# Optimization experiments

Hardware: AMD Instinct MI355X
Metric: run time of the kernel (lower is better)

Reference implementation:

```python
import jax, jax.numpy as jnp
import numpy as np

N_NODES = 50000
N_EDGES = 600000
F_IN = 128
HID = 128
N_CLASSES = 10


def _gcn_graph(edge_index, n_nodes):
    # PyG GCNConv: add self-loops, deg computed on target (col) with weight 1,
    # norm_e = deg^-1/2[src] * deg^-1/2[dst]
    src = jnp.concatenate([edge_index[0], jnp.arange(n_nodes, dtype=edge_index.dtype)])
    dst = jnp.concatenate([edge_index[1], jnp.arange(n_nodes, dtype=edge_index.dtype)])
    deg = jax.ops.segment_sum(jnp.ones_like(dst, dtype=jnp.float32), dst, num_segments=n_nodes)
    dinv = jnp.where(deg > 0, jax.lax.rsqrt(deg), 0.0)
    norm = dinv[src] * dinv[dst]  # [E+N]
    return src, dst, norm


def _gcn_layer(x, W, b, src, dst, norm, n_nodes):
    h = x @ W                      # [N, out] linear first (bias applied post-agg)
    m = h[src] * norm[:, None]     # gather + scale, [E+N, out]
    out = jax.ops.segment_sum(m, dst, num_segments=n_nodes)  # scatter-add
    return out + b


def setup_inputs() -> dict:
    key = jax.random.key(0)
    ks = jax.random.split(key, 4)
    x = jax.random.normal(ks[0], (N_NODES, F_IN), dtype=jnp.float32)
    edge_index = jax.random.randint(ks[1], (2, N_EDGES), 0, N_NODES, dtype=jnp.int64)
    # Glorot-ish init scale for weights
    W_stack = jax.random.normal(ks[2], (8, HID, HID), dtype=jnp.float32) * (1.0 / np.sqrt(HID))
    b_stack = jnp.zeros((8, HID), dtype=jnp.float32)
    W_out = jax.random.normal(ks[3], (HID, N_CLASSES), dtype=jnp.float32) * (1.0 / np.sqrt(HID))
    b_out = jnp.zeros((N_CLASSES,), dtype=jnp.float32)
    return {"x": x, "edge_index": edge_index, "W_stack": W_stack, "b_stack": b_stack,
            "W_out": W_out, "b_out": b_out}


def reference(x, edge_index, W_stack, b_stack, W_out, b_out):
    n_nodes = x.shape[0]
    src, dst, norm = _gcn_graph(edge_index, n_nodes)
    h = x
    for i in range(8):  # conv1..conv8 with ELU
        h = jax.nn.elu(_gcn_layer(h, W_stack[i], b_stack[i], src, dst, norm, n_nodes))
    # conv9: no activation
    return _gcn_layer(h, W_out, b_out, src, dst, norm, n_nodes)
```

## Files before the change

### kernel.cpp

```cpp
#include <hip/hip_runtime.h>
#include <math.h>

#define NN 50000
#define NE 600000
#define HID 128
#define NCLS 10
#define T2S 16

typedef __bf16 bf16x8 __attribute__((ext_vector_type(8)));
typedef float f32x16 __attribute__((ext_vector_type(16)));

__device__ __forceinline__ void split3(float f, ushort& h, ushort& m, ushort& l) {
    unsigned uh = __float_as_uint(f) & 0xffff0000u;
    float fm = f - __uint_as_float(uh);
    unsigned um = __float_as_uint(fm) & 0xffff0000u;
    float fl = fm - __uint_as_float(um);
    h = (ushort)(uh >> 16);
    m = (ushort)(um >> 16);
    l = (ushort)(__float_as_uint(fl) >> 16);
}


__global__ __launch_bounds__(256) void k_count(const int* __restrict__ edge,
                                               int* __restrict__ counts) {
    int e = blockIdx.x * 256 + threadIdx.x;
    if (e < NE) atomicAdd(&counts[edge[NE + e]], 1);
}

__device__ __forceinline__ int wave_incl_scan(int x, int lane) {
#pragma unroll
    for (int off = 1; off < 64; off <<= 1) {
        int y = __shfl_up(x, off, 64);
        if (lane >= off) x += y;
    }
    return x;
}

__global__ __launch_bounds__(256) void k_scan1(const int* __restrict__ counts,
                                               int* __restrict__ rowptr,
                                               int* __restrict__ bsum,
                                               float* __restrict__ dinv) {
    __shared__ int ws[4];
    int tid = threadIdx.x;
    int i = blockIdx.x * 256 + tid;
    int lane = tid & 63, wv = tid >> 6;
    int v = (i < NN) ? counts[i] : 0;
    if (i < NN) dinv[i] = rsqrtf((float)(v + 1));
    int x = wave_incl_scan(v, lane);
    if (lane == 63) ws[wv] = x;
    __syncthreads();
    int off = 0;
    for (int j = 0; j < wv; ++j) off += ws[j];
    if (i < NN) rowptr[i] = off + x - v;
    if (tid == 255) bsum[blockIdx.x] = off + x;
}

__global__ __launch_bounds__(256) void k_scan2(int* __restrict__ bsum, int n) {
    __shared__ int ws[4];
    int tid = threadIdx.x;
    int lane = tid & 63, wv = tid >> 6;
    int v = (tid < n) ? bsum[tid] : 0;
    int x = wave_incl_scan(v, lane);
    if (lane == 63) ws[wv] = x;
    __syncthreads();
    int off = 0;
    for (int j = 0; j < wv; ++j) off += ws[j];
    __syncthreads();
    if (tid < n) bsum[tid] = off + x - v;
}

__global__ __launch_bounds__(256) void k_scan3(int* __restrict__ rowptr,
                                               const int* __restrict__ bsum) {
    int i = blockIdx.x * 256 + threadIdx.x;
    if (i < NN) rowptr[i] += bsum[blockIdx.x];
    if (i == 0) rowptr[NN] = NE;
}

__global__ __launch_bounds__(256) void k_fill(const int* __restrict__ edge,
                                              const int* __restrict__ rowptr,
                                              int* __restrict__ cursor,
                                              const float* __restrict__ dinv,
                                              int2* __restrict__ csr) {
    int e = blockIdx.x * 256 + threadIdx.x;
    if (e >= NE) return;
    int s = edge[e], d = edge[NE + e];
    int slot = atomicSub(&cursor[d], 1) - 1;
    csr[rowptr[d] + slot] = make_int2(s, __float_as_int(dinv[s] * dinv[d]));
}


__global__ __launch_bounds__(256) void k_split_w(const float* __restrict__ Wst,
                                                 ushort* __restrict__ Wt4) {
    int i = blockIdx.x * 256 + threadIdx.x;
    if (i >= 8 * HID * HID) return;
    int l = i >> 14;
    int k = (i >> 7) & 127;
    int n = i & 127;
    ushort h, m, lo;
    split3(Wst[i], h, m, lo);
    int ks = k >> 4, r = k & 15;
    size_t base = ((((size_t)l * 3) * 8 + ks) * 128 + n) * 16 + r;
    const size_t pstride = (size_t)8 * 128 * 16;
    Wt4[base] = h;
    Wt4[base + pstride] = m;
    Wt4[base + 2 * pstride] = lo;
}


__global__ __launch_bounds__(256) void k_mfma_gemm(const float* __restrict__ H,
                                                   const ushort* __restrict__ Wt,
                                                   float* __restrict__ T) {
    int tid = threadIdx.x;
    int lane = tid & 63, w = tid >> 6;
    int l31 = lane & 31, lh = lane >> 5;
    int rowbase = blockIdx.x * 128;

    int grow = rowbase + w * 32 + l31;
    if (grow >= NN) grow = NN - 1;
    const float* arow = H + (size_t)grow * HID + lh * 8;
    const ushort* wbase = Wt + (size_t)l31 * 16 + lh * 8;

    f32x16 acc[4] = {};

#pragma unroll 2
    for (int s = 0; s < 8; ++s) {
        const float4* ap = (const float4*)(arow + s * 16);
        float4 f0 = ap[0], f1 = ap[1];
        float av[8] = {f0.x, f0.y, f0.z, f0.w, f1.x, f1.y, f1.z, f1.w};
        union { ushort u[8]; bf16x8 v; } ah, am, al;
#pragma unroll
        for (int q = 0; q < 8; ++q) split3(av[q], ah.u[q], am.u[q], al.u[q]);

        uint4 bf[3][4];
#pragma unroll
        for (int p = 0; p < 3; ++p)
#pragma unroll
            for (int c = 0; c < 4; ++c)
                bf[p][c] = *(const uint4*)(wbase + (((size_t)p * 8 + s) * 128 + c * 32) * 16);

#pragma unroll
        for (int c = 0; c < 4; ++c)
            acc[c] = __builtin_amdgcn_mfma_f32_32x32x16_bf16(ah.v, *(const bf16x8*)&bf[0][c], acc[c], 0, 0, 0);
#pragma unroll
        for (int c = 0; c < 4; ++c)
            acc[c] = __builtin_amdgcn_mfma_f32_32x32x16_bf16(ah.v, *(const bf16x8*)&bf[1][c], acc[c], 0, 0, 0);
#pragma unroll
        for (int c = 0; c < 4; ++c)
            acc[c] = __builtin_amdgcn_mfma_f32_32x32x16_bf16(am.v, *(const bf16x8*)&bf[0][c], acc[c], 0, 0, 0);
#pragma unroll
        for (int c = 0; c < 4; ++c)
            acc[c] = __builtin_amdgcn_mfma_f32_32x32x16_bf16(ah.v, *(const bf16x8*)&bf[2][c], acc[c], 0, 0, 0);
#pragma unroll
        for (int c = 0; c < 4; ++c)
            acc[c] = __builtin_amdgcn_mfma_f32_32x32x16_bf16(am.v, *(const bf16x8*)&bf[1][c], acc[c], 0, 0, 0);
#pragma unroll
        for (int c = 0; c < 4; ++c)
            acc[c] = __builtin_amdgcn_mfma_f32_32x32x16_bf16(al.v, *(const bf16x8*)&bf[0][c], acc[c], 0, 0, 0);
    }

#pragma unroll
    for (int c = 0; c < 4; ++c)
#pragma unroll
        for (int reg = 0; reg < 16; ++reg) {
            int r = (reg & 3) + 8 * (reg >> 2) + 4 * lh;
            int gr = rowbase + w * 32 + r;
            if (gr < NN)
                T[(size_t)gr * HID + c * 32 + l31] = acc[c][reg];
        }
}

__device__ __forceinline__ void gather2_to_lds(const float* __restrict__ Tin,
                                               const int* __restrict__ rowptr,
                                               const int2* __restrict__ csr,
                                               const float* __restrict__ dinv,
                                               float4 bv, float* Hs,
                                               int rowbase, int w, int h, int l31) {
    int lrow = w * 16 + h;
    int node = rowbase + lrow;
    if (node >= NN) node = NN - 1;
    int beg = rowptr[node], end = rowptr[node + 1];
    float sn = dinv[node];
    float4 tv = ((const float4*)(Tin + (size_t)node * HID))[l31];

    for (int i = 0; i < 8; ++i) {
        int nlrow = lrow + 2;
        int nbeg = 0, nend = 0;
        float nsn = 0.f;
        float4 ntv = {0.f, 0.f, 0.f, 0.f};
        if (i < 7) {
            int nnode = rowbase + nlrow;
            if (nnode >= NN) nnode = NN - 1;
            nbeg = rowptr[nnode];
            nend = rowptr[nnode + 1];
            nsn = dinv[nnode];
            ntv = ((const float4*)(Tin + (size_t)nnode * HID))[l31];
        }

        float s2 = sn * sn;
        float4 acc;
        acc.x = s2 * tv.x + bv.x;
        acc.y = s2 * tv.y + bv.y;
        acc.z = s2 * tv.z + bv.z;
        acc.w = s2 * tv.w + bv.w;

        const int2 zed = make_int2(0, 0);
        int p = beg;
        int2 e0 = (p < end) ? csr[p] : zed;
        int2 e1 = (p + 1 < end) ? csr[p + 1] : zed;
        int2 e2 = (p + 2 < end) ? csr[p + 2] : zed;
        int2 e3 = (p + 3 < end) ? csr[p + 3] : zed;
        for (; p < end; p += 4) {
            float4 u0 = ((const float4*)(Tin + (size_t)e0.x * HID))[l31];
            float4 u1 = ((const float4*)(Tin + (size_t)e1.x * HID))[l31];
            float4 u2 = ((const float4*)(Tin + (size_t)e2.x * HID))[l31];
            float4 u3 = ((const float4*)(Tin + (size_t)e3.x * HID))[l31];
            float w0 = __int_as_float(e0.y), w1 = __int_as_float(e1.y);
            float w2 = __int_as_float(e2.y), w3 = __int_as_float(e3.y);
            e0 = (p + 4 < end) ? csr[p + 4] : zed;
            e1 = (p + 5 < end) ? csr[p + 5] : zed;
            e2 = (p + 6 < end) ? csr[p + 6] : zed;
            e3 = (p + 7 < end) ? csr[p + 7] : zed;
            acc.x += w0 * u0.x; acc.y += w0 * u0.y; acc.z += w0 * u0.z; acc.w += w0 * u0.w;
            acc.x += w1 * u1.x; acc.y += w1 * u1.y; acc.z += w1 * u1.z; acc.w += w1 * u1.w;
            acc.x += w2 * u2.x; acc.y += w2 * u2.y; acc.z += w2 * u2.z; acc.w += w2 * u2.w;
            acc.x += w3 * u3.x; acc.y += w3 * u3.y; acc.z += w3 * u3.z; acc.w += w3 * u3.w;
        }

        acc.x = acc.x > 0.f ? acc.x : expm1f(acc.x);
        acc.y = acc.y > 0.f ? acc.y : expm1f(acc.y);
        acc.z = acc.z > 0.f ? acc.z : expm1f(acc.z);
        acc.w = acc.w > 0.f ? acc.w : expm1f(acc.w);
        int byte = lrow * 512 + l31 * 16;
        byte ^= (lrow & 7) << 4;
        *(float4*)((char*)Hs + byte) = acc;

        lrow = nlrow; beg = nbeg; end = nend; sn = nsn; tv = ntv;
    }
}


__global__ __launch_bounds__(256, 4) void k_fused(const float* __restrict__ Tin,
                                                  const ushort* __restrict__ Wt,
                                                  const int* __restrict__ rowptr,
                                                  const int2* __restrict__ csr,
                                                  const float* __restrict__ dinv,
                                                  const float* __restrict__ bias,
                                                  float* __restrict__ Tout) {
    __shared__ float Hs[64 * 128];
    int tid = threadIdx.x;
    int lane = tid & 63, w = tid >> 6;
    int hh = lane >> 5, l31 = lane & 31;
    int rowbase = blockIdx.x * 64;

    float4 bv = ((const float4*)bias)[l31];

    gather2_to_lds(Tin, rowptr, csr, dinv, bv, Hs, rowbase, w, hh, l31);
    __syncthreads();

    int lh = hh;
    int rloc = (w >> 1) * 32 + l31;
    int colh = w & 1;
    const ushort* wbase = Wt + ((size_t)(colh * 64) + l31) * 16 + lh * 8;

    f32x16 acc2[2] = {};

#pragma unroll 2
    for (int s = 0; s < 8; ++s) {
        int byte = rloc * 512 + s * 64 + lh * 32;
        int sw = (rloc & 7) << 4;
        float4 f0 = *(const float4*)((const char*)Hs + (byte ^ sw));
        float4 f1 = *(const float4*)((const char*)Hs + ((byte + 16) ^ sw));
        float av[8] = {f0.x, f0.y, f0.z, f0.w, f1.x, f1.y, f1.z, f1.w};
        union { ushort u[8]; bf16x8 v; } ah, am, al;
#pragma unroll
        for (int q = 0; q < 8; ++q) split3(av[q], ah.u[q], am.u[q], al.u[q]);

        uint4 bf[3][2];
#pragma unroll
        for (int p = 0; p < 3; ++p)
#pragma unroll
            for (int c = 0; c < 2; ++c)
                bf[p][c] = *(const uint4*)(wbase + (((size_t)p * 8 + s) * 128 + c * 32) * 16);

#pragma unroll
        for (int c = 0; c < 2; ++c)
            acc2[c] = __builtin_amdgcn_mfma_f32_32x32x16_bf16(ah.v, *(const bf16x8*)&bf[0][c], acc2[c], 0, 0, 0);
#pragma unroll
        for (int c = 0; c < 2; ++c)
            acc2[c] = __builtin_amdgcn_mfma_f32_32x32x16_bf16(ah.v, *(const bf16x8*)&bf[1][c], acc2[c], 0, 0, 0);
#pragma unroll
        for (int c = 0; c < 2; ++c)
            acc2[c] = __builtin_amdgcn_mfma_f32_32x32x16_bf16(am.v, *(const bf16x8*)&bf[0][c], acc2[c], 0, 0, 0);
#pragma unroll
        for (int c = 0; c < 2; ++c)
            acc2[c] = __builtin_amdgcn_mfma_f32_32x32x16_bf16(ah.v, *(const bf16x8*)&bf[2][c], acc2[c], 0, 0, 0);
#pragma unroll
        for (int c = 0; c < 2; ++c)
            acc2[c] = __builtin_amdgcn_mfma_f32_32x32x16_bf16(am.v, *(const bf16x8*)&bf[1][c], acc2[c], 0, 0, 0);
#pragma unroll
        for (int c = 0; c < 2; ++c)
            acc2[c] = __builtin_amdgcn_mfma_f32_32x32x16_bf16(al.v, *(const bf16x8*)&bf[0][c], acc2[c], 0, 0, 0);
    }

#pragma unroll
    for (int c = 0; c < 2; ++c)
#pragma unroll
        for (int reg = 0; reg < 16; ++reg) {
            int r = (reg & 3) + 8 * (reg >> 2) + 4 * lh;
            int gr = rowbase + (w >> 1) * 32 + r;
            if (gr < NN)
                Tout[(size_t)gr * HID + colh * 64 + c * 32 + l31] = acc2[c][reg];
        }
}


__global__ __launch_bounds__(256, 4) void k_fused_out(const float* __restrict__ Tin,
                                                      const float* __restrict__ W,
                                                      const int* __restrict__ rowptr,
                                                      const int2* __restrict__ csr,
                                                      const float* __restrict__ dinv,
                                                      const float* __restrict__ bias,
                                                      float* __restrict__ T2) {
    __shared__ float Hs[64 * 128];
    __shared__ float Ws[128 * 11];
    int tid = threadIdx.x;
    int lane = tid & 63, w = tid >> 6;
    int hh = lane >> 5, l31 = lane & 31;
    int rowbase = blockIdx.x * 64;

    for (int m = tid; m < HID * NCLS; m += 256) {
        int k = m / NCLS, c = m - k * NCLS;
        Ws[k * 11 + c] = W[m];
    }

    float4 bv = ((const float4*)bias)[l31];
    gather2_to_lds(Tin, rowptr, csr, dinv, bv, Hs, rowbase, w, hh, l31);
    __syncthreads();

    int row = tid >> 2;
    int t4 = tid & 3;
    float acc[NCLS];
#pragma unroll
    for (int c = 0; c < NCLS; ++c) acc[c] = 0.f;
    int sw = (row & 7) << 4;
#pragma unroll
    for (int q = 0; q < 8; ++q) {
        int c16 = q * 4 + t4;
        float4 f = *(const float4*)((const char*)Hs + ((row * 512 + c16 * 16) ^ sw));
        float hv[4] = {f.x, f.y, f.z, f.w};
#pragma unroll
        for (int j = 0; j < 4; ++j) {
            const float* wr = &Ws[(c16 * 4 + j) * 11];
#pragma unroll
            for (int c = 0; c < NCLS; ++c) acc[c] += hv[j] * wr[c];
        }
    }
#pragma unroll
    for (int off = 2; off >= 1; off >>= 1) {
#pragma unroll
        for (int c = 0; c < NCLS; ++c) acc[c] += __shfl_xor(acc[c], off, 4);
    }
    int gr = rowbase + row;
    if (t4 == 0 && gr < NN) {
#pragma unroll
        for (int c = 0; c < NCLS; ++c) T2[(size_t)gr * T2S + c] = acc[c];
    }
}

__global__ __launch_bounds__(256) void k_gather_out(const float* __restrict__ T2,
                                                    float* __restrict__ out,
                                                    const int* __restrict__ rowptr,
                                                    const int2* __restrict__ csr,
                                                    const float* __restrict__ dinv,
                                                    const float* __restrict__ bias) {
    int lane = threadIdx.x & 63;
    int node = (blockIdx.x * 256 + threadIdx.x) >> 6;
    if (node >= NN) return;
    int slot = lane >> 4, c = lane & 15;
    int beg = rowptr[node], end = rowptr[node + 1];
    float acc = 0.f;
    if (c < NCLS) {
        for (int i = beg + slot; i < end; i += 4) {
            int2 e = csr[i];
            acc += __int_as_float(e.y) * T2[(size_t)e.x * T2S + c];
        }
    }
    acc += __shfl_xor(acc, 16, 64);
    acc += __shfl_xor(acc, 32, 64);
    if (slot == 0 && c < NCLS) {
        float sn = dinv[node];
        sn *= sn;
        out[node * NCLS + c] = acc + sn * T2[(size_t)node * T2S + c] + bias[c];
    }
}


extern "C" void kernel_launch(void* const* d_in, const int* in_sizes, int n_in,
                              void* d_out, int out_size, void* d_ws, size_t ws_size,
                              hipStream_t stream) {
    (void)in_sizes; (void)n_in; (void)out_size; (void)ws_size;
    const float* x       = (const float*)d_in[0];
    const int*   edge    = (const int*)d_in[1];
    const float* W_stack = (const float*)d_in[2];
    const float* b_stack = (const float*)d_in[3];
    const float* W_out   = (const float*)d_in[4];
    const float* b_out   = (const float*)d_in[5];
    float* out = (float*)d_out;

    char* ws = (char*)d_ws;
    const size_t bigbuf = (size_t)NN * HID * sizeof(float);
    float* X      = (float*)ws;
    float* Y      = (float*)(ws + bigbuf);
    char*  p      = ws + 2 * bigbuf;
    int2*  csr    = (int2*)p;              p += sizeof(int2) * NE;
    float* dinv   = (float*)p;             p += sizeof(float) * NN;
    int*   rowptr = (int*)p;               p += sizeof(int) * (NN + 1);
    int*   counts = (int*)p;               p += sizeof(int) * NN;
    int*   bsum   = (int*)p;               p += sizeof(int) * 256;
    p = (char*)(((size_t)p + 15) & ~(size_t)15);
    ushort* Wt4 = (ushort*)p;  p += sizeof(ushort) * 8 * 3 * HID * HID;
    float* T2b  = (float*)p;   p += sizeof(float) * NN * T2S;

    const int NB_N  = (NN + 255) / 256;
    const int NB_E  = (NE + 255) / 256;
    const int NB_G  = (NN + 127) / 128;
    const int NB_F  = (NN + 63) / 64;
    const int NB_A  = (NN * 64 + 255) / 256;
    const int NB_SW = (8 * HID * HID + 255) / 256;

    hipMemsetAsync(counts, 0, sizeof(int) * NN, stream);
    k_count<<<NB_E, 256, 0, stream>>>(edge, counts);
    k_scan1<<<NB_N, 256, 0, stream>>>(counts, rowptr, bsum, dinv);
    k_scan2<<<1, 256, 0, stream>>>(bsum, NB_N);
    k_scan3<<<NB_N, 256, 0, stream>>>(rowptr, bsum);
    k_fill<<<NB_E, 256, 0, stream>>>(edge, rowptr, counts, dinv, csr);

    k_split_w<<<NB_SW, 256, 0, stream>>>(W_stack, Wt4);

    k_mfma_gemm<<<NB_G, 256, 0, stream>>>(x, Wt4, Y);

    float* cur = Y;
    float* nxt = X;
    for (int l = 0; l < 7; ++l) {
        k_fused<<<NB_F, 256, 0, stream>>>(cur, Wt4 + (size_t)(l + 1) * 3 * HID * HID,
                                          rowptr, csr, dinv,
                                          b_stack + (size_t)l * HID, nxt);
        float* t = cur; cur = nxt; nxt = t;
    }

    k_fused_out<<<NB_F, 256, 0, stream>>>(cur, W_out, rowptr, csr, dinv,
                                          b_stack + (size_t)7 * HID, T2b);

    k_gather_out<<<NB_A, 256, 0, stream>>>(T2b, out, rowptr, csr, dinv, b_out);
}
```

Before: 649.6 us.

## Fuse all GCN layers into one cooperative persistent kernel with grid syncs

Replaces the chain of per-layer launches (first GEMM, seven fused gather+GEMM layers, output layer, final gather) with a single cooperative kernel of 782 blocks that uses grid.sync between layers. The first GEMM is re-tiled to 64-row tiles to match the fused layout. The goal is to remove kernel launch gaps and tail effects between the roughly ten dependent kernels. The cost is that cooperative launch needs all 782 blocks co-resident, which at 4 blocks per CU relies on register and LDS limits. If the launch fails, it falls back to the multi-kernel path.

New measurement: 1.617 ms. +148.9%, slower.

```diff
diff --git a/kernel.cpp b/kernel.cpp
--- a/kernel.cpp
+++ b/kernel.cpp
@@ -1,11 +1,15 @@
 #include <hip/hip_runtime.h>
+#include <hip/hip_cooperative_groups.h>
 #include <math.h>
+
+namespace cg = cooperative_groups;
 
 #define NN 50000
 #define NE 600000
 #define HID 128
 #define NCLS 10
 #define T2S 16
+#define NBF 782
 
 typedef __bf16 bf16x8 __attribute__((ext_vector_type(8)));
 typedef float f32x16 __attribute__((ext_vector_type(16)));
@@ -106,68 +110,6 @@
     Wt4[base + 2 * pstride] = lo;
 }
 
-
-__global__ __launch_bounds__(256) void k_mfma_gemm(const float* __restrict__ H,
-                                                   const ushort* __restrict__ Wt,
-                                                   float* __restrict__ T) {
-    int tid = threadIdx.x;
-    int lane = tid & 63, w = tid >> 6;
-    int l31 = lane & 31, lh = lane >> 5;
-    int rowbase = blockIdx.x * 128;
-
-    int grow = rowbase + w * 32 + l31;
-    if (grow >= NN) grow = NN - 1;
-    const float* arow = H + (size_t)grow * HID + lh * 8;
-    const ushort* wbase = Wt + (size_t)l31 * 16 + lh * 8;
-
-    f32x16 acc[4] = {};
-
-#pragma unroll 2
-    for (int s = 0; s < 8; ++s) {
-        const float4* ap = (const float4*)(arow + s * 16);
-        float4 f0 = ap[0], f1 = ap[1];
-        float av[8] = {f0.x, f0.y, f0.z, f0.w, f1.x, f1.y, f1.z, f1.w};
-        union { ushort u[8]; bf16x8 v; } ah, am, al;
-#pragma unroll
-        for (int q = 0; q < 8; ++q) split3(av[q], ah.u[q], am.u[q], al.u[q]);
-
-        uint4 bf[3][4];
-#pragma unroll
-        for (int p = 0; p < 3; ++p)
-#pragma unroll
-            for (int c = 0; c < 4; ++c)
-                bf[p][c] = *(const uint4*)(wbase + (((size_t)p * 8 + s) * 128 + c * 32) * 16);
-
-#pragma unroll
-        for (int c = 0; c < 4; ++c)
-            acc[c] = __builtin_amdgcn_mfma_f32_32x32x16_bf16(ah.v, *(const bf16x8*)&bf[0][c], acc[c], 0, 0, 0);
-#pragma unroll
-        for (int c = 0; c < 4; ++c)
-            acc[c] = __builtin_amdgcn_mfma_f32_32x32x16_bf16(ah.v, *(const bf16x8*)&bf[1][c], acc[c], 0, 0, 0);
-#pragma unroll
-        for (int c = 0; c < 4; ++c)
-            acc[c] = __builtin_amdgcn_mfma_f32_32x32x16_bf16(am.v, *(const bf16x8*)&bf[0][c], acc[c], 0, 0, 0);
-#pragma unroll
-        for (int c = 0; c < 4; ++c)
-            acc[c] = __builtin_amdgcn_mfma_f32_32x32x16_bf16(ah.v, *(const bf16x8*)&bf[2][c], acc[c], 0, 0, 0);
-#pragma unroll
-        for (int c = 0; c < 4; ++c)
-            acc[c] = __builtin_amdgcn_mfma_f32_32x32x16_bf16(am.v, *(const bf16x8*)&bf[1][c], acc[c], 0, 0, 0);
-#pragma unroll
-        for (int c = 0; c < 4; ++c)
-            acc[c] = __builtin_amdgcn_mfma_f32_32x32x16_bf16(al.v, *(const bf16x8*)&bf[0][c], acc[c], 0, 0, 0);
-    }
-
-#pragma unroll
-    for (int c = 0; c < 4; ++c)
-#pragma unroll
-        for (int reg = 0; reg < 16; ++reg) {
-            int r = (reg & 3) + 8 * (reg >> 2) + 4 * lh;
-            int gr = rowbase + w * 32 + r;
-            if (gr < NN)
-                T[(size_t)gr * HID + c * 32 + l31] = acc[c][reg];
-        }
-}
 
 __device__ __forceinline__ void gather2_to_lds(const float* __restrict__ Tin,
                                                const int* __restrict__ rowptr,
@@ -238,6 +180,217 @@
     }
 }
 
+__device__ __forceinline__ void mfma_step(const float av[8],
+                                          const ushort* __restrict__ wbase,
+                                          int s, f32x16 acc2[2]) {
+    union { ushort u[8]; bf16x8 v; } ah, am, al;
+#pragma unroll
+    for (int q = 0; q < 8; ++q) split3(av[q], ah.u[q], am.u[q], al.u[q]);
+
+    uint4 bf[3][2];
+#pragma unroll
+    for (int p = 0; p < 3; ++p)
+#pragma unroll
+        for (int c = 0; c < 2; ++c)
+            bf[p][c] = *(const uint4*)(wbase + (((size_t)p * 8 + s) * 128 + c * 32) * 16);
+
+#pragma unroll
+    for (int c = 0; c < 2; ++c)
+        acc2[c] = __builtin_amdgcn_mfma_f32_32x32x16_bf16(ah.v, *(const bf16x8*)&bf[0][c], acc2[c], 0, 0, 0);
+#pragma unroll
+    for (int c = 0; c < 2; ++c)
+        acc2[c] = __builtin_amdgcn_mfma_f32_32x32x16_bf16(ah.v, *(const bf16x8*)&bf[1][c], acc2[c], 0, 0, 0);
+#pragma unroll
+    for (int c = 0; c < 2; ++c)
+        acc2[c] = __builtin_amdgcn_mfma_f32_32x32x16_bf16(am.v, *(const bf16x8*)&bf[0][c], acc2[c], 0, 0, 0);
+#pragma unroll
+    for (int c = 0; c < 2; ++c)
+        acc2[c] = __builtin_amdgcn_mfma_f32_32x32x16_bf16(ah.v, *(const bf16x8*)&bf[2][c], acc2[c], 0, 0, 0);
+#pragma unroll
+    for (int c = 0; c < 2; ++c)
+        acc2[c] = __builtin_amdgcn_mfma_f32_32x32x16_bf16(am.v, *(const bf16x8*)&bf[1][c], acc2[c], 0, 0, 0);
+#pragma unroll
+    for (int c = 0; c < 2; ++c)
+        acc2[c] = __builtin_amdgcn_mfma_f32_32x32x16_bf16(al.v, *(const bf16x8*)&bf[0][c], acc2[c], 0, 0, 0);
+}
+
+__device__ __forceinline__ void cstore(f32x16 acc2[2], float* __restrict__ Tout,
+                                       int rowbase, int w, int lh, int l31, int colh) {
+#pragma unroll
+    for (int c = 0; c < 2; ++c)
+#pragma unroll
+        for (int reg = 0; reg < 16; ++reg) {
+            int r = (reg & 3) + 8 * (reg >> 2) + 4 * lh;
+            int gr = rowbase + (w >> 1) * 32 + r;
+            if (gr < NN)
+                Tout[(size_t)gr * HID + colh * 64 + c * 32 + l31] = acc2[c][reg];
+        }
+}
+
+__device__ __forceinline__ void phase2_gemm(const float* Hs,
+                                            const ushort* __restrict__ Wt,
+                                            float* __restrict__ Tout,
+                                            int rowbase, int tid) {
+    int lane = tid & 63, w = tid >> 6;
+    int l31 = lane & 31, lh = lane >> 5;
+    int rloc = (w >> 1) * 32 + l31;
+    int colh = w & 1;
+    const ushort* wbase = Wt + ((size_t)(colh * 64) + l31) * 16 + lh * 8;
+
+    f32x16 acc2[2] = {};
+#pragma unroll 2
+    for (int s = 0; s < 8; ++s) {
+        int byte = rloc * 512 + s * 64 + lh * 32;
+        int sw = (rloc & 7) << 4;
+        float4 f0 = *(const float4*)((const char*)Hs + (byte ^ sw));
+        float4 f1 = *(const float4*)((const char*)Hs + ((byte + 16) ^ sw));
+        float av[8] = {f0.x, f0.y, f0.z, f0.w, f1.x, f1.y, f1.z, f1.w};
+        mfma_step(av, wbase, s, acc2);
+    }
+    cstore(acc2, Tout, rowbase, w, lh, l31, colh);
+}
+
+__device__ __forceinline__ void gemm0_tile(const float* __restrict__ x,
+                                           const ushort* __restrict__ Wt,
+                                           float* __restrict__ Tout,
+                                           int rowbase, int tid) {
+    int lane = tid & 63, w = tid >> 6;
+    int l31 = lane & 31, lh = lane >> 5;
+    int rloc = (w >> 1) * 32 + l31;
+    int colh = w & 1;
+    int grow = rowbase + rloc;
+    if (grow >= NN) grow = NN - 1;
+    const float* arow = x + (size_t)grow * HID + lh * 8;
+    const ushort* wbase = Wt + ((size_t)(colh * 64) + l31) * 16 + lh * 8;
+
+    f32x16 acc2[2] = {};
+#pragma unroll 2
+    for (int s = 0; s < 8; ++s) {
+        const float4* ap = (const float4*)(arow + s * 16);
+        float4 f0 = ap[0], f1 = ap[1];
+        float av[8] = {f0.x, f0.y, f0.z, f0.w, f1.x, f1.y, f1.z, f1.w};
+        mfma_step(av, wbase, s, acc2);
+    }
+    cstore(acc2, Tout, rowbase, w, lh, l31, colh);
+}
+
+__device__ __forceinline__ void fusedout_phase2(const float* Hs, const float* Ws,
+                                                float* __restrict__ T2,
+                                                int rowbase, int tid) {
+    int row = tid >> 2;
+    int t4 = tid & 3;
+    float acc[NCLS];
+#pragma unroll
+    for (int c = 0; c < NCLS; ++c) acc[c] = 0.f;
+    int sw = (row & 7) << 4;
+#pragma unroll
+    for (int q = 0; q < 8; ++q) {
+        int c16 = q * 4 + t4;
+        float4 f = *(const float4*)((const char*)Hs + ((row * 512 + c16 * 16) ^ sw));
+        float hv[4] = {f.x, f.y, f.z, f.w};
+#pragma unroll
+        for (int j = 0; j < 4; ++j) {
+            const float* wr = &Ws[(c16 * 4 + j) * 11];
+#pragma unroll
+            for (int c = 0; c < NCLS; ++c) acc[c] += hv[j] * wr[c];
+        }
+    }
+#pragma unroll
+    for (int off = 2; off >= 1; off >>= 1) {
+#pragma unroll
+        for (int c = 0; c < NCLS; ++c) acc[c] += __shfl_xor(acc[c], off, 4);
+    }
+    int gr = rowbase + row;
+    if (t4 == 0 && gr < NN) {
+#pragma unroll
+        for (int c = 0; c < NCLS; ++c) T2[(size_t)gr * T2S + c] = acc[c];
+    }
+}
+
+__device__ __forceinline__ void gatherout_body(const float* __restrict__ T2,
+                                               float* __restrict__ out,
+                                               const int* __restrict__ rowptr,
+                                               const int2* __restrict__ csr,
+                                               const float* __restrict__ dinv,
+                                               const float* __restrict__ bias,
+                                               int node, int lane) {
+    if (node >= NN) return;
+    int slot = lane >> 4, c = lane & 15;
+    int beg = rowptr[node], end = rowptr[node + 1];
+    float acc = 0.f;
+    if (c < NCLS) {
+        for (int i = beg + slot; i < end; i += 4) {
+            int2 e = csr[i];
+            acc += __int_as_float(e.y) * T2[(size_t)e.x * T2S + c];
+        }
+    }
+    acc += __shfl_xor(acc, 16, 64);
+    acc += __shfl_xor(acc, 32, 64);
+    if (slot == 0 && c < NCLS) {
+        float sn = dinv[node];
+        sn *= sn;
+        out[node * NCLS + c] = acc + sn * T2[(size_t)node * T2S + c] + bias[c];
+    }
+}
+
+
+__global__ __launch_bounds__(256, 4) void k_mega(const float* __restrict__ x,
+                                                 const ushort* __restrict__ Wt4,
+                                                 const float* __restrict__ W_out,
+                                                 const int* __restrict__ rowptr,
+                                                 const int2* __restrict__ csr,
+                                                 const float* __restrict__ dinv,
+                                                 const float* __restrict__ b_stack,
+                                                 const float* __restrict__ b_out,
+                                                 float* __restrict__ Y,
+                                                 float* __restrict__ X,
+                                                 float* __restrict__ T2b,
+                                                 float* __restrict__ out) {
+    __shared__ float Hs[64 * 128];
+    __shared__ float Ws[128 * 11];
+    cg::grid_group grid = cg::this_grid();
+    int tid = threadIdx.x;
+    int rowbase = blockIdx.x * 64;
+    int lane = tid & 63, w = tid >> 6;
+    int hh = lane >> 5, l31 = lane & 31;
+
+    gemm0_tile(x, Wt4, Y, rowbase, tid);
+    grid.sync();
+
+    float* cur = Y;
+    float* nxt = X;
+    for (int l = 0; l < 7; ++l) {
+        float4 bv = ((const float4*)(b_stack + (size_t)l * HID))[l31];
+        gather2_to_lds(cur, rowptr, csr, dinv, bv, Hs, rowbase, w, hh, l31);
+        __syncthreads();
+        phase2_gemm(Hs, Wt4 + (size_t)(l + 1) * 3 * HID * HID, nxt, rowbase, tid);
+        grid.sync();
+        float* t = cur; cur = nxt; nxt = t;
+    }
+
+    for (int m = tid; m < HID * NCLS; m += 256) {
+        int k = m / NCLS, c = m - k * NCLS;
+        Ws[k * 11 + c] = W_out[m];
+    }
+    {
+        float4 bv = ((const float4*)(b_stack + (size_t)7 * HID))[l31];
+        gather2_to_lds(cur, rowptr, csr, dinv, bv, Hs, rowbase, w, hh, l31);
+    }
+    __syncthreads();
+    fusedout_phase2(Hs, Ws, T2b, rowbase, tid);
+    grid.sync();
+
+    for (int base = blockIdx.x * 4; base < NN; base += NBF * 4) {
+        gatherout_body(T2b, out, rowptr, csr, dinv, b_out, base + (tid >> 6), lane);
+    }
+}
+
+
+__global__ __launch_bounds__(256) void k_gemm0(const float* __restrict__ x,
+                                               const ushort* __restrict__ Wt,
+                                               float* __restrict__ T) {
+    gemm0_tile(x, Wt, T, blockIdx.x * 64, threadIdx.x);
+}
 
 __global__ __launch_bounds__(256, 4) void k_fused(const float* __restrict__ Tin,
                                                   const ushort* __restrict__ Wt,
@@ -251,68 +404,11 @@
     int lane = tid & 63, w = tid >> 6;
     int hh = lane >> 5, l31 = lane & 31;
     int rowbase = blockIdx.x * 64;
-
     float4 bv = ((const float4*)bias)[l31];
-
     gather2_to_lds(Tin, rowptr, csr, dinv, bv, Hs, rowbase, w, hh, l31);
     __syncthreads();
-
-    int lh = hh;
-    int rloc = (w >> 1) * 32 + l31;
-    int colh = w & 1;
-    const ushort* wbase = Wt + ((size_t)(colh * 64) + l31) * 16 + lh * 8;
-
-    f32x16 acc2[2] = {};
-
-#pragma unroll 2
-    for (int s = 0; s < 8; ++s) {
-        int byte = rloc * 512 + s * 64 + lh * 32;
-        int sw = (rloc & 7) << 4;
-        float4 f0 = *(const float4*)((const char*)Hs + (byte ^ sw));
-        float4 f1 = *(const float4*)((const char*)Hs + ((byte + 16) ^ sw));
-        float av[8] = {f0.x, f0.y, f0.z, f0.w, f1.x, f1.y, f1.z, f1.w};
-        union { ushort u[8]; bf16x8 v; } ah, am, al;
-#pragma unroll
-        for (int q = 0; q < 8; ++q) split3(av[q], ah.u[q], am.u[q], al.u[q]);
-
-        uint4 bf[3][2];
-#pragma unroll
-        for (int p = 0; p < 3; ++p)
-#pragma unroll
-            for (int c = 0; c < 2; ++c)
-                bf[p][c] = *(const uint4*)(wbase + (((size_t)p * 8 + s) * 128 + c * 32) * 16);
-
-#pragma unroll
-        for (int c = 0; c < 2; ++c)
-            acc2[c] = __builtin_amdgcn_mfma_f32_32x32x16_bf16(ah.v, *(const bf16x8*)&bf[0][c], acc2[c], 0, 0, 0);
-#pragma unroll
-        for (int c = 0; c < 2; ++c)
-            acc2[c] = __builtin_amdgcn_mfma_f32_32x32x16_bf16(ah.v, *(const bf16x8*)&bf[1][c], acc2[c], 0, 0, 0);
-#pragma unroll
-        for (int c = 0; c < 2; ++c)
-            acc2[c] = __builtin_amdgcn_mfma_f32_32x32x16_bf16(am.v, *(const bf16x8*)&bf[0][c], acc2[c], 0, 0, 0);
-#pragma unroll
-        for (int c = 0; c < 2; ++c)
-            acc2[c] = __builtin_amdgcn_mfma_f32_32x32x16_bf16(ah.v, *(const bf16x8*)&bf[2][c], acc2[c], 0, 0, 0);
-#pragma unroll
-        for (int c = 0; c < 2; ++c)
-            acc2[c] = __builtin_amdgcn_mfma_f32_32x32x16_bf16(am.v, *(const bf16x8*)&bf[1][c], acc2[c], 0, 0, 0);
-#pragma unroll
-        for (int c = 0; c < 2; ++c)
-            acc2[c] = __builtin_amdgcn_mfma_f32_32x32x16_bf16(al.v, *(const bf16x8*)&bf[0][c], acc2[c], 0, 0, 0);
-    }
-
-#pragma unroll
-    for (int c = 0; c < 2; ++c)
-#pragma unroll
-        for (int reg = 0; reg < 16; ++reg) {
-            int r = (reg & 3) + 8 * (reg >> 2) + 4 * lh;
-            int gr = rowbase + (w >> 1) * 32 + r;
-            if (gr < NN)
-                Tout[(size_t)gr * HID + colh * 64 + c * 32 + l31] = acc2[c][reg];
-        }
-}
-
+    phase2_gemm(Hs, Wt, Tout, rowbase, tid);
+}
 
 __global__ __launch_bounds__(256, 4) void k_fused_out(const float* __restrict__ Tin,
                                                       const float* __restrict__ W,
@@ -327,44 +423,14 @@
     int lane = tid & 63, w = tid >> 6;
     int hh = lane >> 5, l31 = lane & 31;
     int rowbase = blockIdx.x * 64;
-
     for (int m = tid; m < HID * NCLS; m += 256) {
         int k = m / NCLS, c = m - k * NCLS;
         Ws[k * 11 + c] = W[m];
     }
-
     float4 bv = ((const float4*)bias)[l31];
     gather2_to_lds(Tin, rowptr, csr, dinv, bv, Hs, rowbase, w, hh, l31);
     __syncthreads();
-
-    int row = tid >> 2;
-    int t4 = tid & 3;
-    float acc[NCLS];
-#pragma unroll
-    for (int c = 0; c < NCLS; ++c) acc[c] = 0.f;
-    int sw = (row & 7) << 4;
-#pragma unroll
-    for (int q = 0; q < 8; ++q) {
-        int c16 = q * 4 + t4;
-        float4 f = *(const float4*)((const char*)Hs + ((row * 512 + c16 * 16) ^ sw));
-        float hv[4] = {f.x, f.y, f.z, f.w};
-#pragma unroll
-        for (int j = 0; j < 4; ++j) {
-            const float* wr = &Ws[(c16 * 4 + j) * 11];
-#pragma unroll
-            for (int c = 0; c < NCLS; ++c) acc[c] += hv[j] * wr[c];
-        }
-    }
-#pragma unroll
-    for (int off = 2; off >= 1; off >>= 1) {
-#pragma unroll
-        for (int c = 0; c < NCLS; ++c) acc[c] += __shfl_xor(acc[c], off, 4);
-    }
-    int gr = rowbase + row;
-    if (t4 == 0 && gr < NN) {
-#pragma unroll
-        for (int c = 0; c < NCLS; ++c) T2[(size_t)gr * T2S + c] = acc[c];
-    }
+    fusedout_phase2(Hs, Ws, T2, rowbase, tid);
 }
 
 __global__ __launch_bounds__(256) void k_gather_out(const float* __restrict__ T2,
@@ -375,23 +441,7 @@
                                                     const float* __restrict__ bias) {
     int lane = threadIdx.x & 63;
     int node = (blockIdx.x * 256 + threadIdx.x) >> 6;
-    if (node >= NN) return;
-    int slot = lane >> 4, c = lane & 15;
-    int beg = rowptr[node], end = rowptr[node + 1];
-    float acc = 0.f;
-    if (c < NCLS) {
-        for (int i = beg + slot; i < end; i += 4) {
-            int2 e = csr[i];
-            acc += __int_as_float(e.y) * T2[(size_t)e.x * T2S + c];
-        }
-    }
-    acc += __shfl_xor(acc, 16, 64);
-    acc += __shfl_xor(acc, 32, 64);
-    if (slot == 0 && c < NCLS) {
-        float sn = dinv[node];
-        sn *= sn;
-        out[node * NCLS + c] = acc + sn * T2[(size_t)node * T2S + c] + bias[c];
-    }
+    gatherout_body(T2, out, rowptr, csr, dinv, bias, node, lane);
 }
 
 
@@ -423,8 +473,6 @@
 
     const int NB_N  = (NN + 255) / 256;
     const int NB_E  = (NE + 255) / 256;
-    const int NB_G  = (NN + 127) / 128;
-    const int NB_F  = (NN + 63) / 64;
     const int NB_A  = (NN * 64 + 255) / 256;
     const int NB_SW = (8 * HID * HID + 255) / 256;
 
@@ -437,19 +485,27 @@
 
     k_split_w<<<NB_SW, 256, 0, stream>>>(W_stack, Wt4);
 
-    k_mfma_gemm<<<NB_G, 256, 0, stream>>>(x, Wt4, Y);
-
+    {
+        void* args[] = {(void*)&x, (void*)&Wt4, (void*)&W_out, (void*)&rowptr,
+                        (void*)&csr, (void*)&dinv, (void*)&b_stack, (void*)&b_out,
+                        (void*)&Y, (void*)&X, (void*)&T2b, (void*)&out};
+        hipError_t err = hipLaunchCooperativeKernel((const void*)k_mega,
+                                                    dim3(NBF), dim3(256),
+                                                    args, 0, stream);
+        if (err == hipSuccess) return;
+        (void)hipGetLastError();
+    }
+
+    k_gemm0<<<NBF, 256, 0, stream>>>(x, Wt4, Y);
     float* cur = Y;
     float* nxt = X;
     for (int l = 0; l < 7; ++l) {
-        k_fused<<<NB_F, 256, 0, stream>>>(cur, Wt4 + (size_t)(l + 1) * 3 * HID * HID,
-                                          rowptr, csr, dinv,
-                                          b_stack + (size_t)l * HID, nxt);
+        k_fused<<<NBF, 256, 0, stream>>>(cur, Wt4 + (size_t)(l + 1) * 3 * HID * HID,
+                                         rowptr, csr, dinv,
+                                         b_stack + (size_t)l * HID, nxt);
         float* t = cur; cur = nxt; nxt = t;
     }
-
-    k_fused_out<<<NB_F, 256, 0, stream>>>(cur, W_out, rowptr, csr, dinv,
-                                          b_stack + (size_t)7 * HID, T2b);
-
+    k_fused_out<<<NBF, 256, 0, stream>>>(cur, W_out, rowptr, csr, dinv,
+                                         b_stack + (size_t)7 * HID, T2b);
     k_gather_out<<<NB_A, 256, 0, stream>>>(T2b, out, rowptr, csr, dinv, b_out);
 }
```
